# Kernel optimization log

Measured on AMD Instinct MI355X. Metric: run time of the kernel, lower is better.

The kernel has to match this reference:

```python
import jax, jax.numpy as jnp
import numpy as np

N_NODES = 50000
N_EDGES = 800000
N_REL = 12
D_IN = 768
D_H = 128
N_GRAPHS = 64


def _rgcn_layer(x, src, dst, etype, W, W_root, b):
    # PyG RGCNConv (default aggr='mean', root_weight=True, bias=True):
    # out = x @ W_root + b + sum_r scatter_mean_{e: type(e)=r}( x[src_e] @ W[r] -> dst_e )
    n = x.shape[0]
    out = x @ W_root + b
    for r in range(W.shape[0]):  # small fixed loop over 12 relations
        h = x @ W[r]                                   # [N, H]
        m = (etype == r)                               # [E]
        msg = jnp.where(m[:, None], h[src], 0.0)       # [E, H]
        s = jax.ops.segment_sum(msg, dst, num_segments=n)
        cnt = jax.ops.segment_sum(m.astype(x.dtype), dst, num_segments=n)
        out = out + s / jnp.maximum(cnt, 1.0)[:, None]
    return out


def setup_inputs() -> dict:
    key = jax.random.key(0)
    ks = jax.random.split(key, 24)
    inp = {
        "x": jax.random.normal(ks[0], (N_NODES, D_IN), dtype=jnp.float32),
        "edge_index": jax.random.randint(ks[1], (2, N_EDGES), 0, N_NODES, dtype=jnp.int32),
        "edge_type": jax.random.randint(ks[2], (N_EDGES,), 0, N_REL, dtype=jnp.int32),
        "batch": jnp.sort(jax.random.randint(ks[3], (N_NODES,), 0, N_GRAPHS, dtype=jnp.int32)),
        "inds_head": jax.random.randint(ks[4], (N_GRAPHS,), 0, 10, dtype=jnp.int32),
        "inds_tail": jax.random.randint(ks[5], (N_GRAPHS,), 0, 10, dtype=jnp.int32),
    }
    dims = [D_IN] + [D_H] * 4  # 5 layers
    for i, din in enumerate(dims):
        inp[f"W{i}"] = 0.02 * jax.random.normal(ks[6 + 3 * i], (N_REL, din, D_H), dtype=jnp.float32)
        inp[f"R{i}"] = 0.02 * jax.random.normal(ks[7 + 3 * i], (din, D_H), dtype=jnp.float32)
        inp[f"B{i}"] = jnp.zeros((D_H,), dtype=jnp.float32)
    return inp


def reference(x, edge_index, edge_type, batch, inds_head, inds_tail,
              W0, R0, B0, W1, R1, B1, W2, R2, B2, W3, R3, B3, W4, R4, B4):
    src, dst = edge_index[0], edge_index[1]
    params = [(W0, R0, B0), (W1, R1, B1), (W2, R2, B2), (W3, R3, B3), (W4, R4, B4)]
    h = x
    for (W, Wr, b) in params[:-1]:
        h = jax.nn.relu(_rgcn_layer(h, src, dst, edge_type, W, Wr, b))
    W, Wr, b = params[-1]
    h = _rgcn_layer(h, src, dst, edge_type, W, Wr, b)
    # convert per-graph local indices to global node indices via cumulative counts
    counts = jax.ops.segment_sum(jnp.ones_like(batch), batch, num_segments=N_GRAPHS)
    offsets = jnp.concatenate([jnp.zeros((1,), counts.dtype), jnp.cumsum(counts)[:-1]])
    head = h[inds_head + offsets]
    tail = h[inds_tail + offsets]
    return jnp.concatenate([head, tail], axis=-1)  # [B, 2*H]
```

## Files before the change

kernel.cpp:

```cpp
#include <hip/hip_runtime.h>
#include <hip/hip_bf16.h>


#define N_NODES 50000
#define N_EDGES 800000
#define N_REL   12
#define D_IN    768
#define D_H     128
#define N_GRAPH 64

#define BMM   128
#define KSTEP 32
#define LDC   136

typedef _Float16 f16x8 __attribute__((ext_vector_type(8)));
typedef _Float16 f16x4 __attribute__((ext_vector_type(4)));
typedef float    f32x4v __attribute__((ext_vector_type(4)));
typedef unsigned int u32x4 __attribute__((ext_vector_type(4)));

#define GLDS16(g, l) __builtin_amdgcn_global_load_lds( \
    (const __attribute__((address_space(1))) unsigned int*)(g), \
    (__attribute__((address_space(3))) unsigned int*)(l), 16, 0, 0)

__global__ __launch_bounds__(256) void split_f32(
    const float* __restrict__ in, _Float16* __restrict__ hi,
    _Float16* __restrict__ lo, int n4)
{
  int i = blockIdx.x * 256 + threadIdx.x;
  if (i >= n4) return;
  float4 v = *(const float4*)(in + (size_t)i * 4);
  f16x4 h, l;
  h[0] = (_Float16)v.x; l[0] = (_Float16)(v.x - (float)h[0]);
  h[1] = (_Float16)v.y; l[1] = (_Float16)(v.y - (float)h[1]);
  h[2] = (_Float16)v.z; l[2] = (_Float16)(v.z - (float)h[2]);
  h[3] = (_Float16)v.w; l[3] = (_Float16)(v.w - (float)h[3]);
  *(f16x4*)(hi + (size_t)i * 4) = h;
  *(f16x4*)(lo + (size_t)i * 4) = l;
}

__global__ __launch_bounds__(256) void wsplit(
    const float* __restrict__ W, const float* __restrict__ Rm,
    _Float16* __restrict__ th, int K)
{
  int idx = blockIdx.x * 256 + threadIdx.x;
  int total = 13 * 128 * K;
  if (idx >= total) return;
  int z = idx / (128 * K);
  int rem = idx - z * 128 * K;
  int n = rem / K;
  int k = rem - n * K;
  float v = (z < N_REL) ? W[((size_t)z * K + k) * 128 + n] : Rm[(size_t)k * 128 + n];
  th[idx] = (_Float16)v;
}

__global__ __launch_bounds__(256, 4) void gemm_mfma(
    const _Float16* __restrict__ Ah, const _Float16* __restrict__ Al,
    const _Float16* __restrict__ Wh,
    const float* __restrict__ bias,
    _Float16* __restrict__ Hc,
    float* __restrict__ Cden,
    int M, int K, int r0, int rc, int zdim, int nwg)
{
  __shared__ _Float16 lds[3 * BMM * KSTEP];
  _Float16* Ah_s = lds;
  _Float16* Al_s = lds + BMM * KSTEP;
  _Float16* B_s  = lds + 2 * BMM * KSTEP;

  int b = blockIdx.x;
  int q = nwg >> 3, rr = nwg & 7;
  int xcd = b & 7, ix = b >> 3;
  int wg = (xcd < rr ? xcd * (q + 1) : rr * (q + 1) + (xcd - rr) * q) + ix;
  int mt = wg / zdim;
  int z  = wg - mt * zdim;
  const bool is_root = (z >= rc);
  const int m0 = mt * BMM;

  const _Float16* __restrict__ b_src =
      Wh + (size_t)(is_root ? N_REL : (r0 + z)) * 128 * K;

  const int t = threadIdx.x;
  const int lane = t & 63;
  const int wave = t >> 6;
  const int wr = wave >> 1, wc = wave & 1;
  const int l16 = lane & 15, kq = lane >> 4;

  const int c0 = wave * 128 + lane;
  const int c1 = c0 + 64;
  const int cr0 = c0 >> 2, cs0 = (c0 & 3) << 3;
  const int cr1 = c1 >> 2, cs1 = (c1 & 3) << 3;
  int a0 = m0 + cr0; a0 = a0 < M ? a0 : M - 1;
  int a1 = m0 + cr1; a1 = a1 < M ? a1 : M - 1;
  const _Float16* gAh0 = Ah + (size_t)a0 * K + cs0;
  const _Float16* gAh1 = Ah + (size_t)a1 * K + cs1;
  const _Float16* gAl0 = Al + (size_t)a0 * K + cs0;
  const _Float16* gAl1 = Al + (size_t)a1 * K + cs1;
  const _Float16* gB0  = b_src + (size_t)cr0 * K + cs0;
  const _Float16* gB1  = b_src + (size_t)cr1 * K + cs1;
  _Float16* dAh = Ah_s + wave * 1024;
  _Float16* dAl = Al_s + wave * 1024;
  _Float16* dB  = B_s  + wave * 1024;

  f32x4v acc[4][4];
#pragma unroll
  for (int i = 0; i < 4; ++i)
#pragma unroll
    for (int j = 0; j < 4; ++j) acc[i][j] = (f32x4v){0.f, 0.f, 0.f, 0.f};

  for (int k0 = 0; k0 < K; k0 += KSTEP) {
    GLDS16(gAh0 + k0, dAh);
    GLDS16(gAh1 + k0, dAh + 512);
    GLDS16(gAl0 + k0, dAl);
    GLDS16(gAl1 + k0, dAl + 512);
    GLDS16(gB0  + k0, dB);
    GLDS16(gB1  + k0, dB + 512);
    __syncthreads();

    f16x8 fah[4], fal[4], fb[4];
#pragma unroll
    for (int i = 0; i < 4; ++i) {
      int ra = (wr * 64 + i * 16 + l16) * KSTEP + kq * 8;
      fah[i] = *(const f16x8*)&Ah_s[ra];
      fal[i] = *(const f16x8*)&Al_s[ra];
      int rb = (wc * 64 + i * 16 + l16) * KSTEP + kq * 8;
      fb[i]  = *(const f16x8*)&B_s[rb];
    }
#pragma unroll
    for (int i = 0; i < 4; ++i)
#pragma unroll
      for (int j = 0; j < 4; ++j) {
        acc[i][j] = __builtin_amdgcn_mfma_f32_16x16x32_f16(fah[i], fb[j], acc[i][j], 0, 0, 0);
        acc[i][j] = __builtin_amdgcn_mfma_f32_16x16x32_f16(fal[i], fb[j], acc[i][j], 0, 0, 0);
      }
    __syncthreads();
  }

  if (is_root) {
#pragma unroll
    for (int j = 0; j < 4; ++j) {
      int col = wc * 64 + j * 16 + l16;
      float bv = bias[col];
#pragma unroll
      for (int i = 0; i < 4; ++i)
#pragma unroll
        for (int rg = 0; rg < 4; ++rg) {
          int grow = m0 + wr * 64 + i * 16 + kq * 4 + rg;
          if (grow < M)
            __builtin_nontemporal_store(acc[i][j][rg] + bv,
                                        Cden + (size_t)grow * 128 + col);
        }
    }
  } else {
    _Float16* Cs = lds;
    _Float16* __restrict__ Crel = Hc + (size_t)z * M * 128;
#pragma unroll
    for (int h = 0; h < 2; ++h) {
      if (wr == h) {
#pragma unroll
        for (int i = 0; i < 4; ++i)
#pragma unroll
          for (int j = 0; j < 4; ++j)
#pragma unroll
            for (int rg = 0; rg < 4; ++rg)
              Cs[(i * 16 + kq * 4 + rg) * LDC + wc * 64 + j * 16 + l16] =
                  (_Float16)acc[i][j][rg];
      }
      __syncthreads();
#pragma unroll
      for (int p = 0; p < 4; ++p) {
        int q2 = t + 256 * p;
        int row = q2 >> 4, c16 = (q2 & 15) * 8;
        int gr = m0 + h * 64 + row;
        if (gr < M) {
          u32x4 v = *(const u32x4*)&Cs[row * LDC + c16];
          __builtin_nontemporal_store(v, (u32x4*)(Crel + (size_t)gr * 128 + c16));
        }
      }
      __syncthreads();
    }
  }
}

__global__ void count_edges(const int* __restrict__ ei, const int* __restrict__ et,
                            int* __restrict__ deg, int* __restrict__ cnt) {
  int e = blockIdx.x * 256 + threadIdx.x;
  if (e >= N_EDGES) return;
  int d = ei[N_EDGES + e];
  int r = et[e];
  atomicAdd(&deg[d], 1);
  atomicAdd(&cnt[r * N_NODES + d], 1);
}

__global__ void inv_counts(const int* __restrict__ cnt, float* __restrict__ inv) {
  int i = blockIdx.x * 256 + threadIdx.x;
  if (i < N_REL * N_NODES) {
    int c = cnt[i];
    inv[i] = 1.0f / (float)(c > 1 ? c : 1);
  }
}

__global__ __launch_bounds__(1024) void scan_deg(const int* __restrict__ deg,
                                                 int* __restrict__ row_ptr,
                                                 int* __restrict__ cursor) {
  __shared__ int buf[1024];
  __shared__ int carry;
  if (threadIdx.x == 0) carry = 0;
  __syncthreads();
  for (int base = 0; base < N_NODES; base += 1024) {
    int i = base + threadIdx.x;
    int x = (i < N_NODES) ? deg[i] : 0;
    buf[threadIdx.x] = x;
    __syncthreads();
#pragma unroll
    for (int off = 1; off < 1024; off <<= 1) {
      int t = (threadIdx.x >= off) ? buf[threadIdx.x - off] : 0;
      __syncthreads();
      buf[threadIdx.x] += t;
      __syncthreads();
    }
    int incl = buf[threadIdx.x];
    int excl = incl - x;
    if (i < N_NODES) {
      int rp = carry + excl;
      row_ptr[i] = rp;
      cursor[i] = rp;
    }
    __syncthreads();
    if (threadIdx.x == 1023) carry += incl;
    __syncthreads();
  }
  if (threadIdx.x == 0) row_ptr[N_NODES] = carry;
}

__global__ void scatter_edges(const int* __restrict__ ei, const int* __restrict__ et,
                              const float* __restrict__ inv,
                              int* __restrict__ cursor,
                              unsigned long long* __restrict__ csr_ow) {
  int e = blockIdx.x * 256 + threadIdx.x;
  if (e >= N_EDGES) return;
  int s = ei[e];
  int d = ei[N_EDGES + e];
  int r = et[e];
  int pos = atomicAdd(&cursor[d], 1);
  unsigned off = ((unsigned)r * (unsigned)N_NODES + (unsigned)s) * 256u;
  float w = inv[r * N_NODES + d];
  union { float f; unsigned u; } wu; wu.f = w;
  csr_ow[pos] = (unsigned long long)off | ((unsigned long long)wu.u << 32);
}

__global__ void count_graphs(const int* __restrict__ batch, int* __restrict__ gcnt) {
  int i = blockIdx.x * 256 + threadIdx.x;
  if (i < N_NODES) atomicAdd(&gcnt[batch[i]], 1);
}

__global__ __launch_bounds__(256) void aggregate(
    const _Float16* __restrict__ Hc,
    const int* __restrict__ row_ptr,
    const unsigned long long* __restrict__ csr_ow,
    float* __restrict__ h,
    _Float16* __restrict__ AhO, _Float16* __restrict__ AlO,
    int r0, int rc, int do_relu, int write_split, int write_f32)
{
  const int v = blockIdx.x * 4 + (threadIdx.x >> 6);
  if (v >= N_NODES) return;
  const int lane = threadIdx.x & 63;
  float2 acc = *(const float2*)&h[(size_t)v * 128 + lane * 2];
  const int e0 = row_ptr[v];
  const int e1 = row_ptr[v + 1];
  const bool full = (rc == N_REL);
  const char* __restrict__ HcB = (const char*)Hc;

  for (int base = e0; base < e1; base += 64) {
    int n = e1 - base; n = n < 64 ? n : 64;
    int idx = base + lane; idx = idx < e1 ? idx : e1 - 1;
    unsigned long long ow = csr_ow[idx];
    unsigned off_l = (unsigned)ow;
    float w_l = __uint_as_float((unsigned)(ow >> 32));
    for (int i = 0; i < n; ++i) {
      unsigned off = (unsigned)__shfl((int)off_l, i);
      float w = __shfl(w_l, i);
      if (!full) {
        unsigned rowi = off >> 8;
        unsigned r = rowi / (unsigned)N_NODES;
        if (r - (unsigned)r0 >= (unsigned)rc) continue;
        off -= (unsigned)r0 * (unsigned)N_NODES * 256u;
      }
      unsigned pv = *((const unsigned*)(HcB + off) + lane);
      union { unsigned u; _Float16 f[2]; } cv; cv.u = pv;
      acc.x += w * (float)cv.f[0];
      acc.y += w * (float)cv.f[1];
    }
  }
  if (do_relu) { acc.x = fmaxf(acc.x, 0.f); acc.y = fmaxf(acc.y, 0.f); }
  if (write_split) {
    union { _Float16 f[2]; unsigned u; } ph, pl;
    ph.f[0] = (_Float16)acc.x; ph.f[1] = (_Float16)acc.y;
    pl.f[0] = (_Float16)(acc.x - (float)ph.f[0]);
    pl.f[1] = (_Float16)(acc.y - (float)ph.f[1]);
    ((unsigned*)AhO)[(size_t)v * 64 + lane] = ph.u;
    ((unsigned*)AlO)[(size_t)v * 64 + lane] = pl.u;
  }
  if (write_f32) *(float2*)&h[(size_t)v * 128 + lane * 2] = acc;
}

__global__ __launch_bounds__(256) void final_gather(
    const float* __restrict__ h, const int* __restrict__ gcnt,
    const int* __restrict__ ih, const int* __restrict__ it,
    float* __restrict__ out)
{
  __shared__ int off_s;
  int g = blockIdx.x;
  if (threadIdx.x == 0) {
    int off = 0;
    for (int j = 0; j < g; ++j) off += gcnt[j];
    off_s = off;
  }
  __syncthreads();
  int off = off_s;
  int c = threadIdx.x;
  int hi = ih[g] + off;
  int ti = it[g] + off;
  out[(size_t)g * 256 + c] = (c < D_H) ? h[(size_t)hi * D_H + c]
                                       : h[(size_t)ti * D_H + (c - D_H)];
}

extern "C" void kernel_launch(void* const* d_in, const int* in_sizes, int n_in,
                              void* d_out, int out_size, void* d_ws, size_t ws_size,
                              hipStream_t stream) {
  (void)in_sizes; (void)n_in; (void)out_size;
  const float* x   = (const float*)d_in[0];
  const int* ei    = (const int*)d_in[1];
  const int* et    = (const int*)d_in[2];
  const int* batch = (const int*)d_in[3];
  const int* ih    = (const int*)d_in[4];
  const int* it    = (const int*)d_in[5];
  const float* Wl[5]; const float* Rl[5]; const float* Bl[5];
  for (int l = 0; l < 5; ++l) {
    Wl[l] = (const float*)d_in[6 + 3 * l];
    Rl[l] = (const float*)d_in[7 + 3 * l];
    Bl[l] = (const float*)d_in[8 + 3 * l];
  }

  char* p = (char*)d_ws;
  size_t used = 0;
  auto alloc = [&](size_t bytes) {
    char* r = p;
    size_t rb = (bytes + 255) & ~(size_t)255;
    p += rb; used += rb;
    return r;
  };
  const size_t HREL16 = (size_t)N_NODES * D_H * 2;
  float* h        = (float*)alloc((size_t)N_NODES * D_H * 4);
  _Float16* Ahb   = (_Float16*)alloc((size_t)N_NODES * D_IN * 2);
  _Float16* Alb   = (_Float16*)alloc((size_t)N_NODES * D_IN * 2);
  _Float16* Wh    = (_Float16*)alloc((size_t)13 * 128 * D_IN * 2);
  float* inv      = (float*)alloc((size_t)N_REL * N_NODES * 4);
  int* cnt        = (int*)alloc((size_t)N_REL * N_NODES * 4);
  int* deg        = (int*)alloc((size_t)N_NODES * 4);
  int* rowp       = (int*)alloc((size_t)(N_NODES + 1) * 4);
  int* cursor     = (int*)alloc((size_t)N_NODES * 4);
  unsigned long long* csr_ow = (unsigned long long*)alloc((size_t)N_EDGES * 8);
  int* gcnt       = (int*)alloc((size_t)N_GRAPH * 4);

  size_t remain = (ws_size > used) ? (ws_size - used) : 0;
  int RC = (int)(remain / HREL16);
  if (RC > N_REL) RC = N_REL;
  if (RC < 1) RC = 1;
  _Float16* Hc = (_Float16*)alloc((size_t)RC * HREL16);

  hipMemsetAsync(cnt, 0, (size_t)N_REL * N_NODES * 4, stream);
  hipMemsetAsync(deg, 0, (size_t)N_NODES * 4, stream);
  hipMemsetAsync(gcnt, 0, (size_t)N_GRAPH * 4, stream);

  count_edges<<<(N_EDGES + 255) / 256, 256, 0, stream>>>(ei, et, deg, cnt);
  inv_counts<<<(N_REL * N_NODES + 255) / 256, 256, 0, stream>>>(cnt, inv);
  scan_deg<<<1, 1024, 0, stream>>>(deg, rowp, cursor);
  scatter_edges<<<(N_EDGES + 255) / 256, 256, 0, stream>>>(ei, et, inv, cursor, csr_ow);
  count_graphs<<<(N_NODES + 255) / 256, 256, 0, stream>>>(batch, gcnt);

  int n4 = N_NODES * D_IN / 4;
  split_f32<<<(n4 + 255) / 256, 256, 0, stream>>>(x, Ahb, Alb, n4);

  const int mtiles = (N_NODES + BMM - 1) / BMM;
  for (int l = 0; l < 5; ++l) {
    int K = (l == 0) ? D_IN : D_H;
    int wtot = 13 * 128 * K;
    wsplit<<<(wtot + 255) / 256, 256, 0, stream>>>(Wl[l], Rl[l], Wh, K);

    int nchunks = (N_REL + RC - 1) / RC;
    for (int ch = 0; ch < nchunks; ++ch) {
      int r0 = ch * RC;
      int rc = (N_REL - r0) < RC ? (N_REL - r0) : RC;
      int zdim = rc + (ch == 0 ? 1 : 0);
      int nwg = zdim * mtiles;
      gemm_mfma<<<nwg, 256, 0, stream>>>(Ahb, Alb, Wh, Bl[l], Hc, h,
                                         N_NODES, K, r0, rc, zdim, nwg);
      int final_ch = (ch == nchunks - 1);
      int relu  = (l < 4 && final_ch) ? 1 : 0;
      int wspl  = (l < 4 && final_ch) ? 1 : 0;
      int wf32  = (!final_ch || l == 4) ? 1 : 0;
      aggregate<<<(N_NODES + 3) / 4, 256, 0, stream>>>(Hc, rowp, csr_ow,
                                                       h, Ahb, Alb,
                                                       r0, rc, relu, wspl, wf32);
    }
  }

  final_gather<<<N_GRAPH, 256, 0, stream>>>(h, gcnt, ih, it, (float*)d_out);
}
```

Baseline: 1.642 ms.

## Parallelize degree scan across blocks and unroll aggregate edge gathers

```diff
diff --git a/kernel.cpp b/kernel.cpp
--- a/kernel.cpp
+++ b/kernel.cpp
@@ -12,6 +12,9 @@
 #define BMM   128
 #define KSTEP 32
 #define LDC   136
+
+#define SCAN_B 1024
+#define SCAN_NB ((N_NODES + SCAN_B - 1) / SCAN_B)
 
 typedef _Float16 f16x8 __attribute__((ext_vector_type(8)));
 typedef _Float16 f16x4 __attribute__((ext_vector_type(4)));
@@ -198,37 +201,42 @@
   }
 }
 
-__global__ __launch_bounds__(1024) void scan_deg(const int* __restrict__ deg,
-                                                 int* __restrict__ row_ptr,
-                                                 int* __restrict__ cursor) {
-  __shared__ int buf[1024];
-  __shared__ int carry;
-  if (threadIdx.x == 0) carry = 0;
+__global__ __launch_bounds__(SCAN_B) void scan_local(
+    const int* __restrict__ deg, int* __restrict__ locx, int* __restrict__ bsum) {
+  __shared__ int buf[SCAN_B];
+  int i = blockIdx.x * SCAN_B + threadIdx.x;
+  int x = (i < N_NODES) ? deg[i] : 0;
+  buf[threadIdx.x] = x;
   __syncthreads();
-  for (int base = 0; base < N_NODES; base += 1024) {
-    int i = base + threadIdx.x;
-    int x = (i < N_NODES) ? deg[i] : 0;
-    buf[threadIdx.x] = x;
+#pragma unroll
+  for (int off = 1; off < SCAN_B; off <<= 1) {
+    int t = (threadIdx.x >= off) ? buf[threadIdx.x - off] : 0;
     __syncthreads();
-#pragma unroll
-    for (int off = 1; off < 1024; off <<= 1) {
-      int t = (threadIdx.x >= off) ? buf[threadIdx.x - off] : 0;
-      __syncthreads();
-      buf[threadIdx.x] += t;
-      __syncthreads();
-    }
-    int incl = buf[threadIdx.x];
-    int excl = incl - x;
-    if (i < N_NODES) {
-      int rp = carry + excl;
-      row_ptr[i] = rp;
-      cursor[i] = rp;
-    }
+    buf[threadIdx.x] += t;
     __syncthreads();
-    if (threadIdx.x == 1023) carry += incl;
-    __syncthreads();
-  }
-  if (threadIdx.x == 0) row_ptr[N_NODES] = carry;
+  }
+  if (i < N_NODES) locx[i] = buf[threadIdx.x] - x;
+  if (threadIdx.x == SCAN_B - 1) bsum[blockIdx.x] = buf[threadIdx.x];
+}
+
+__global__ __launch_bounds__(64) void scan_bsums(int* __restrict__ bsum,
+                                                 int* __restrict__ boff) {
+  if (threadIdx.x == 0) {
+    int run = 0;
+    for (int j = 0; j < SCAN_NB; ++j) { boff[j] = run; run += bsum[j]; }
+  }
+}
+
+__global__ __launch_bounds__(SCAN_B) void scan_apply(
+    const int* __restrict__ locx, const int* __restrict__ boff,
+    int* __restrict__ row_ptr, int* __restrict__ cursor) {
+  int i = blockIdx.x * SCAN_B + threadIdx.x;
+  if (i < N_NODES) {
+    int rp = locx[i] + boff[blockIdx.x];
+    row_ptr[i] = rp;
+    cursor[i] = rp;
+  }
+  if (i == 0) row_ptr[N_NODES] = N_EDGES;
 }
 
 __global__ void scatter_edges(const int* __restrict__ ei, const int* __restrict__ et,
@@ -252,6 +260,12 @@
   if (i < N_NODES) atomicAdd(&gcnt[batch[i]], 1);
 }
 
+__device__ inline void fmacc(float2& acc, unsigned pv, float w) {
+  union { unsigned u; _Float16 f[2]; } cv; cv.u = pv;
+  acc.x += w * (float)cv.f[0];
+  acc.y += w * (float)cv.f[1];
+}
+
 __global__ __launch_bounds__(256) void aggregate(
     const _Float16* __restrict__ Hc,
     const int* __restrict__ row_ptr,
@@ -260,36 +274,49 @@
     _Float16* __restrict__ AhO, _Float16* __restrict__ AlO,
     int r0, int rc, int do_relu, int write_split, int write_f32)
 {
-  const int v = blockIdx.x * 4 + (threadIdx.x >> 6);
+  int v = blockIdx.x * 4 + (threadIdx.x >> 6);
+  v = __builtin_amdgcn_readfirstlane(v);
   if (v >= N_NODES) return;
   const int lane = threadIdx.x & 63;
   float2 acc = *(const float2*)&h[(size_t)v * 128 + lane * 2];
   const int e0 = row_ptr[v];
   const int e1 = row_ptr[v + 1];
-  const bool full = (rc == N_REL);
   const char* __restrict__ HcB = (const char*)Hc;
 
-  for (int base = e0; base < e1; base += 64) {
-    int n = e1 - base; n = n < 64 ? n : 64;
-    int idx = base + lane; idx = idx < e1 ? idx : e1 - 1;
-    unsigned long long ow = csr_ow[idx];
-    unsigned off_l = (unsigned)ow;
-    float w_l = __uint_as_float((unsigned)(ow >> 32));
-    for (int i = 0; i < n; ++i) {
-      unsigned off = (unsigned)__shfl((int)off_l, i);
-      float w = __shfl(w_l, i);
-      if (!full) {
-        unsigned rowi = off >> 8;
-        unsigned r = rowi / (unsigned)N_NODES;
-        if (r - (unsigned)r0 >= (unsigned)rc) continue;
-        off -= (unsigned)r0 * (unsigned)N_NODES * 256u;
-      }
-      unsigned pv = *((const unsigned*)(HcB + off) + lane);
-      union { unsigned u; _Float16 f[2]; } cv; cv.u = pv;
-      acc.x += w * (float)cv.f[0];
-      acc.y += w * (float)cv.f[1];
-    }
-  }
+  if (rc == N_REL) {
+    int i = e0;
+    for (; i + 4 <= e1; i += 4) {
+      unsigned long long d0 = csr_ow[i + 0];
+      unsigned long long d1 = csr_ow[i + 1];
+      unsigned long long d2 = csr_ow[i + 2];
+      unsigned long long d3 = csr_ow[i + 3];
+      unsigned p0 = *((const unsigned*)(HcB + (unsigned)d0) + lane);
+      unsigned p1 = *((const unsigned*)(HcB + (unsigned)d1) + lane);
+      unsigned p2 = *((const unsigned*)(HcB + (unsigned)d2) + lane);
+      unsigned p3 = *((const unsigned*)(HcB + (unsigned)d3) + lane);
+      fmacc(acc, p0, __uint_as_float((unsigned)(d0 >> 32)));
+      fmacc(acc, p1, __uint_as_float((unsigned)(d1 >> 32)));
+      fmacc(acc, p2, __uint_as_float((unsigned)(d2 >> 32)));
+      fmacc(acc, p3, __uint_as_float((unsigned)(d3 >> 32)));
+    }
+    for (; i < e1; ++i) {
+      unsigned long long d0 = csr_ow[i];
+      unsigned p0 = *((const unsigned*)(HcB + (unsigned)d0) + lane);
+      fmacc(acc, p0, __uint_as_float((unsigned)(d0 >> 32)));
+    }
+  } else {
+    for (int i = e0; i < e1; ++i) {
+      unsigned long long d0 = csr_ow[i];
+      unsigned off = (unsigned)d0;
+      unsigned rowi = off >> 8;
+      unsigned r = rowi / (unsigned)N_NODES;
+      if (r - (unsigned)r0 >= (unsigned)rc) continue;
+      off -= (unsigned)r0 * (unsigned)N_NODES * 256u;
+      unsigned p0 = *((const unsigned*)(HcB + off) + lane);
+      fmacc(acc, p0, __uint_as_float((unsigned)(d0 >> 32)));
+    }
+  }
+
   if (do_relu) { acc.x = fmaxf(acc.x, 0.f); acc.y = fmaxf(acc.y, 0.f); }
   if (write_split) {
     union { _Float16 f[2]; unsigned u; } ph, pl;
@@ -358,6 +385,9 @@
   int* deg        = (int*)alloc((size_t)N_NODES * 4);
   int* rowp       = (int*)alloc((size_t)(N_NODES + 1) * 4);
   int* cursor     = (int*)alloc((size_t)N_NODES * 4);
+  int* locx       = (int*)alloc((size_t)N_NODES * 4);
+  int* bsum       = (int*)alloc((size_t)SCAN_NB * 4);
+  int* boff       = (int*)alloc((size_t)SCAN_NB * 4);
   unsigned long long* csr_ow = (unsigned long long*)alloc((size_t)N_EDGES * 8);
   int* gcnt       = (int*)alloc((size_t)N_GRAPH * 4);
 
@@ -373,7 +403,9 @@
 
   count_edges<<<(N_EDGES + 255) / 256, 256, 0, stream>>>(ei, et, deg, cnt);
   inv_counts<<<(N_REL * N_NODES + 255) / 256, 256, 0, stream>>>(cnt, inv);
-  scan_deg<<<1, 1024, 0, stream>>>(deg, rowp, cursor);
+  scan_local<<<SCAN_NB, SCAN_B, 0, stream>>>(deg, locx, bsum);
+  scan_bsums<<<1, 64, 0, stream>>>(bsum, boff);
+  scan_apply<<<SCAN_NB, SCAN_B, 0, stream>>>(locx, boff, rowp, cursor);
   scatter_edges<<<(N_EDGES + 255) / 256, 256, 0, stream>>>(ei, et, inv, cursor, csr_ow);
   count_graphs<<<(N_NODES + 255) / 256, 256, 0, stream>>>(batch, gcnt);
 
```

Result: faster. 1.371 ms (-16.5%).
